# Performance work log

Measured on AMD Instinct MI355X. Metric: run time of the kernel, lower is better.

The kernel has to match this reference:

```python
import jax, jax.numpy as jnp
import numpy as np

N_NODES = 100000   # n_users + n_items
N_EDGES = 1000000  # avg degree ~10
D = 64             # embed_dim
N_LAYERS = 3


def setup_inputs() -> dict:
    key = jax.random.key(0)
    k1, k2, k3, k4 = jax.random.split(key, 4)
    embedding = jax.random.normal(k1, (N_NODES, D), dtype=jnp.float32)
    src = jax.random.randint(k2, (N_EDGES,), 0, N_NODES)
    dst = jax.random.randint(k3, (N_EDGES,), 0, N_NODES)
    # sqrt_degree is a per-node [N,1] positive scale (1/sqrt(deg) in practice)
    sqrt_degree = jax.random.uniform(k4, (N_NODES, 1), dtype=jnp.float32,
                                     minval=0.01, maxval=1.0)
    return {"embedding": embedding, "sqrt_degree": sqrt_degree,
            "src": src, "dst": dst, "n_layers": N_LAYERS}


def reference(embedding, sqrt_degree, src, dst, n_layers):
    n_nodes = embedding.shape[0]
    h = embedding
    acc = embedding  # ego embedding (layer 0)
    for _ in range(n_layers):
        # Aggregator: scale, copy_src gather, segment-sum scatter, scale
        msg = (h * sqrt_degree)[src]                                   # [E, D]
        h = jax.ops.segment_sum(msg, dst, num_segments=n_nodes)        # [N, D]
        h = h * sqrt_degree
        acc = acc + h
    # torch.mean(torch.stack(all_embed, -1), -1)
    return acc / jnp.asarray(n_layers + 1, dtype=embedding.dtype)
```

## Files before the change

### kernel.cpp

```cpp
#include <hip/hip_runtime.h>
#include <hip/hip_fp16.h>


#define N_NODES 100000
#define D 64
#define ND4 (N_NODES * D / 4)
#define SCAN_B 1024
#define NTILES ((N_NODES + SCAN_B - 1) / SCAN_B)
#define NSLICE 8
#define SLICE_DIV 12500

union H4 { uint2 u; __half2 h[2]; };
union H8 { uint4 u; __half2 h[4]; };

__global__ void init_kernel(const float4* __restrict__ emb,
                            const float* __restrict__ deg,
                            uint2* __restrict__ hs,
                            int* __restrict__ cnt, int n4) {
    int i = blockIdx.x * blockDim.x + threadIdx.x;
    if (i < N_NODES) cnt[i] = 0;
    if (i >= n4) return;
    float dg = deg[i >> 4];
    float4 v = emb[i];
    H4 x;
    x.h[0] = __float22half2_rn(make_float2(v.x * dg, v.y * dg));
    x.h[1] = __float22half2_rn(make_float2(v.z * dg, v.w * dg));
    hs[i] = x.u;
}

__global__ void hist_kernel(const int* __restrict__ dst, int* __restrict__ cnt,
                            int nedges) {
    int e = blockIdx.x * blockDim.x + threadIdx.x;
    if (e < nedges) atomicAdd(&cnt[dst[e]], 1);
}

__global__ void scanA_kernel(const int* __restrict__ cnt, int* __restrict__ off,
                             int* __restrict__ tsum, int n) {
    __shared__ int sm[SCAN_B];
    int t = threadIdx.x;
    int i = blockIdx.x * SCAN_B + t;
    int x = (i < n) ? cnt[i] : 0;
    sm[t] = x;
    __syncthreads();
    for (int o = 1; o < SCAN_B; o <<= 1) {
        int v = (t >= o) ? sm[t - o] : 0;
        __syncthreads();
        sm[t] += v;
        __syncthreads();
    }
    if (i < n) off[i] = sm[t] - x;
    if (t == SCAN_B - 1) tsum[blockIdx.x] = sm[t];
}

__global__ void scanB_kernel(int* __restrict__ tsum, int ntiles) {
    __shared__ int sm[SCAN_B];
    int t = threadIdx.x;
    int x = (t < ntiles) ? tsum[t] : 0;
    sm[t] = x;
    __syncthreads();
    for (int o = 1; o < SCAN_B; o <<= 1) {
        int v = (t >= o) ? sm[t - o] : 0;
        __syncthreads();
        sm[t] += v;
        __syncthreads();
    }
    if (t < ntiles) tsum[t] = sm[t] - x;
}

__global__ void scanC_kernel(int* __restrict__ off, const int* __restrict__ tsum,
                             int* __restrict__ cursor, int n, int nedges) {
    int i = blockIdx.x * blockDim.x + threadIdx.x;
    if (i >= n) return;
    int v = off[i] + tsum[i >> 10];
    off[i] = v;
    cursor[i] = v;
    if (i == 0) off[n] = nedges;
}

__global__ void reorder_kernel(const int* __restrict__ src,
                               const int* __restrict__ dst,
                               int* __restrict__ cursor,
                               int* __restrict__ ssrc, int nedges) {
    int slice = blockIdx.x & (NSLICE - 1);
    int e = (blockIdx.x >> 3) * blockDim.x + threadIdx.x;
    if (e >= nedges) return;
    int d = dst[e];
    if (d / SLICE_DIV != slice) return;
    int p = atomicAdd(&cursor[d], 1);
    ssrc[p] = src[e];
}

__device__ __forceinline__ void acc_h8(float* s, uint4 u) {
    H8 x; x.u = u;
    #pragma unroll
    for (int k = 0; k < 4; ++k) {
        float2 f = __half22float2(x.h[k]);
        s[2 * k]     += f.x;
        s[2 * k + 1] += f.y;
    }
}

__global__ void aggregate_kernel(const uint4* __restrict__ hs_in,
                                 const int* __restrict__ off,
                                 const int* __restrict__ ssrc,
                                 const float* __restrict__ deg,
                                 const float4* __restrict__ acc_in,
                                 float4* __restrict__ acc_out,
                                 uint4* __restrict__ hs_out,
                                 int write_hs, float scale) {
    int tid = blockIdx.x * blockDim.x + threadIdx.x;
    int n = tid >> 3;
    if (n >= N_NODES) return;
    int d8 = tid & 7;
    int start = off[n];
    int end = off[n + 1];
    float s[8] = {0.f, 0.f, 0.f, 0.f, 0.f, 0.f, 0.f, 0.f};

    int j = start;
    for (; j + 4 <= end; j += 4) {
        int ia = ssrc[j];
        int ib = ssrc[j + 1];
        int ic = ssrc[j + 2];
        int id = ssrc[j + 3];
        uint4 va = hs_in[ia * 8 + d8];
        uint4 vb = hs_in[ib * 8 + d8];
        uint4 vc = hs_in[ic * 8 + d8];
        uint4 vd = hs_in[id * 8 + d8];
        acc_h8(s, va);
        acc_h8(s, vb);
        acc_h8(s, vc);
        acc_h8(s, vd);
    }
    for (; j < end; ++j) {
        acc_h8(s, hs_in[ssrc[j] * 8 + d8]);
    }

    float dg = deg[n];
    float t[8];
    #pragma unroll
    for (int k = 0; k < 8; ++k) t[k] = s[k] * dg;

    int base = n * 16 + d8 * 2;
    float4 a0 = acc_in[base];
    float4 a1 = acc_in[base + 1];
    a0.x = (a0.x + t[0]) * scale;
    a0.y = (a0.y + t[1]) * scale;
    a0.z = (a0.z + t[2]) * scale;
    a0.w = (a0.w + t[3]) * scale;
    a1.x = (a1.x + t[4]) * scale;
    a1.y = (a1.y + t[5]) * scale;
    a1.z = (a1.z + t[6]) * scale;
    a1.w = (a1.w + t[7]) * scale;
    acc_out[base] = a0;
    acc_out[base + 1] = a1;

    if (write_hs) {
        H8 o;
        #pragma unroll
        for (int k = 0; k < 4; ++k)
            o.h[k] = __float22half2_rn(
                make_float2(t[2 * k] * dg, t[2 * k + 1] * dg));
        hs_out[tid] = o.u;
    }
}

extern "C" void kernel_launch(void* const* d_in, const int* in_sizes, int n_in,
                              void* d_out, int out_size, void* d_ws, size_t ws_size,
                              hipStream_t stream) {
    const float* emb = (const float*)d_in[0];
    const float* deg = (const float*)d_in[1];
    const int*   src = (const int*)d_in[2];
    const int*   dst = (const int*)d_in[3];
    float* out = (float*)d_out;
    int nedges = in_sizes[2];

    __half* hs_a = (__half*)d_ws;
    __half* hs_b = hs_a + (size_t)N_NODES * D;
    int*   ssrc   = (int*)(hs_b + (size_t)N_NODES * D);
    int*   cnt    = ssrc + nedges;
    int*   off    = cnt + N_NODES;
    int*   cursor = off + N_NODES + 1;
    int*   tsum   = cursor + N_NODES;

    init_kernel<<<(ND4 + 255) / 256, 256, 0, stream>>>(
        (const float4*)emb, deg, (uint2*)hs_a, cnt, ND4);
    hist_kernel<<<(nedges + 255) / 256, 256, 0, stream>>>(dst, cnt, nedges);
    scanA_kernel<<<NTILES, SCAN_B, 0, stream>>>(cnt, off, tsum, N_NODES);
    scanB_kernel<<<1, SCAN_B, 0, stream>>>(tsum, NTILES);
    scanC_kernel<<<(N_NODES + 255) / 256, 256, 0, stream>>>(
        off, tsum, cursor, N_NODES, nedges);
    reorder_kernel<<<NSLICE * ((nedges + 255) / 256), 256, 0, stream>>>(
        src, dst, cursor, ssrc, nedges);

    int nthreads = N_NODES * 8;
    int grid = (nthreads + 255) / 256;
    aggregate_kernel<<<grid, 256, 0, stream>>>(
        (const uint4*)hs_a, off, ssrc, deg, (const float4*)emb,
        (float4*)out, (uint4*)hs_b, 1, 1.0f);
    aggregate_kernel<<<grid, 256, 0, stream>>>(
        (const uint4*)hs_b, off, ssrc, deg, (const float4*)out,
        (float4*)out, (uint4*)hs_a, 1, 1.0f);
    aggregate_kernel<<<grid, 256, 0, stream>>>(
        (const uint4*)hs_a, off, ssrc, deg, (const float4*)out,
        (float4*)out, (uint4*)hs_b, 0, 0.25f);
}
```

Baseline: 259.2 us.

## Record per-edge rank during histogram to drop reorder atomics; add nontemporal hints

```diff
diff --git a/kernel.cpp b/kernel.cpp
--- a/kernel.cpp
+++ b/kernel.cpp
@@ -9,16 +9,27 @@
 #define NTILES ((N_NODES + SCAN_B - 1) / SCAN_B)
 #define NSLICE 8
 #define SLICE_DIV 12500
+#define D_MASK 0x1FFFF
+
+typedef float        f4v __attribute__((ext_vector_type(4)));
+typedef unsigned int u4v __attribute__((ext_vector_type(4)));
 
 union H4 { uint2 u; __half2 h[2]; };
-union H8 { uint4 u; __half2 h[4]; };
-
-__global__ void init_kernel(const float4* __restrict__ emb,
-                            const float* __restrict__ deg,
-                            uint2* __restrict__ hs,
-                            int* __restrict__ cnt, int n4) {
+union H8 { u4v u; __half2 h[4]; };
+
+__global__ void init_hist_kernel(const float4* __restrict__ emb,
+                                 const float* __restrict__ deg,
+                                 const int* __restrict__ dst,
+                                 uint2* __restrict__ hs,
+                                 int* __restrict__ cnt,
+                                 unsigned int* __restrict__ key,
+                                 int n4, int nedges) {
     int i = blockIdx.x * blockDim.x + threadIdx.x;
-    if (i < N_NODES) cnt[i] = 0;
+    if (i < nedges) {
+        int d = dst[i];
+        int r = atomicAdd(&cnt[d], 1);
+        key[i] = (unsigned int)d | ((unsigned int)r << 17);
+    }
     if (i >= n4) return;
     float dg = deg[i >> 4];
     float4 v = emb[i];
@@ -26,12 +37,6 @@
     x.h[0] = __float22half2_rn(make_float2(v.x * dg, v.y * dg));
     x.h[1] = __float22half2_rn(make_float2(v.z * dg, v.w * dg));
     hs[i] = x.u;
-}
-
-__global__ void hist_kernel(const int* __restrict__ dst, int* __restrict__ cnt,
-                            int nedges) {
-    int e = blockIdx.x * blockDim.x + threadIdx.x;
-    if (e < nedges) atomicAdd(&cnt[dst[e]], 1);
 }
 
 __global__ void scanA_kernel(const int* __restrict__ cnt, int* __restrict__ off,
@@ -68,29 +73,29 @@
 }
 
 __global__ void scanC_kernel(int* __restrict__ off, const int* __restrict__ tsum,
-                             int* __restrict__ cursor, int n, int nedges) {
+                             int n, int nedges) {
     int i = blockIdx.x * blockDim.x + threadIdx.x;
     if (i >= n) return;
-    int v = off[i] + tsum[i >> 10];
-    off[i] = v;
-    cursor[i] = v;
+    off[i] += tsum[i >> 10];
     if (i == 0) off[n] = nedges;
 }
 
 __global__ void reorder_kernel(const int* __restrict__ src,
-                               const int* __restrict__ dst,
-                               int* __restrict__ cursor,
+                               const unsigned int* __restrict__ key,
+                               const int* __restrict__ off,
                                int* __restrict__ ssrc, int nedges) {
     int slice = blockIdx.x & (NSLICE - 1);
     int e = (blockIdx.x >> 3) * blockDim.x + threadIdx.x;
     if (e >= nedges) return;
-    int d = dst[e];
+    unsigned int k = __builtin_nontemporal_load(&key[e]);
+    int d = (int)(k & D_MASK);
     if (d / SLICE_DIV != slice) return;
-    int p = atomicAdd(&cursor[d], 1);
-    ssrc[p] = src[e];
-}
-
-__device__ __forceinline__ void acc_h8(float* s, uint4 u) {
+    int r = (int)(k >> 17);
+    int p = off[d] + r;
+    ssrc[p] = __builtin_nontemporal_load(&src[e]);
+}
+
+__device__ __forceinline__ void acc_h8(float* s, u4v u) {
     H8 x; x.u = u;
     #pragma unroll
     for (int k = 0; k < 4; ++k) {
@@ -100,13 +105,13 @@
     }
 }
 
-__global__ void aggregate_kernel(const uint4* __restrict__ hs_in,
+__global__ void aggregate_kernel(const u4v* __restrict__ hs_in,
                                  const int* __restrict__ off,
                                  const int* __restrict__ ssrc,
                                  const float* __restrict__ deg,
-                                 const float4* __restrict__ acc_in,
-                                 float4* __restrict__ acc_out,
-                                 uint4* __restrict__ hs_out,
+                                 const f4v* __restrict__ acc_in,
+                                 f4v* __restrict__ acc_out,
+                                 u4v* __restrict__ hs_out,
                                  int write_hs, float scale) {
     int tid = blockIdx.x * blockDim.x + threadIdx.x;
     int n = tid >> 3;
@@ -117,22 +122,39 @@
     float s[8] = {0.f, 0.f, 0.f, 0.f, 0.f, 0.f, 0.f, 0.f};
 
     int j = start;
+    for (; j + 8 <= end; j += 8) {
+        int i0 = __builtin_nontemporal_load(&ssrc[j]);
+        int i1 = __builtin_nontemporal_load(&ssrc[j + 1]);
+        int i2 = __builtin_nontemporal_load(&ssrc[j + 2]);
+        int i3 = __builtin_nontemporal_load(&ssrc[j + 3]);
+        int i4 = __builtin_nontemporal_load(&ssrc[j + 4]);
+        int i5 = __builtin_nontemporal_load(&ssrc[j + 5]);
+        int i6 = __builtin_nontemporal_load(&ssrc[j + 6]);
+        int i7 = __builtin_nontemporal_load(&ssrc[j + 7]);
+        u4v v0 = hs_in[i0 * 8 + d8];
+        u4v v1 = hs_in[i1 * 8 + d8];
+        u4v v2 = hs_in[i2 * 8 + d8];
+        u4v v3 = hs_in[i3 * 8 + d8];
+        u4v v4 = hs_in[i4 * 8 + d8];
+        u4v v5 = hs_in[i5 * 8 + d8];
+        u4v v6 = hs_in[i6 * 8 + d8];
+        u4v v7 = hs_in[i7 * 8 + d8];
+        acc_h8(s, v0); acc_h8(s, v1); acc_h8(s, v2); acc_h8(s, v3);
+        acc_h8(s, v4); acc_h8(s, v5); acc_h8(s, v6); acc_h8(s, v7);
+    }
     for (; j + 4 <= end; j += 4) {
-        int ia = ssrc[j];
-        int ib = ssrc[j + 1];
-        int ic = ssrc[j + 2];
-        int id = ssrc[j + 3];
-        uint4 va = hs_in[ia * 8 + d8];
-        uint4 vb = hs_in[ib * 8 + d8];
-        uint4 vc = hs_in[ic * 8 + d8];
-        uint4 vd = hs_in[id * 8 + d8];
-        acc_h8(s, va);
-        acc_h8(s, vb);
-        acc_h8(s, vc);
-        acc_h8(s, vd);
+        int i0 = __builtin_nontemporal_load(&ssrc[j]);
+        int i1 = __builtin_nontemporal_load(&ssrc[j + 1]);
+        int i2 = __builtin_nontemporal_load(&ssrc[j + 2]);
+        int i3 = __builtin_nontemporal_load(&ssrc[j + 3]);
+        u4v v0 = hs_in[i0 * 8 + d8];
+        u4v v1 = hs_in[i1 * 8 + d8];
+        u4v v2 = hs_in[i2 * 8 + d8];
+        u4v v3 = hs_in[i3 * 8 + d8];
+        acc_h8(s, v0); acc_h8(s, v1); acc_h8(s, v2); acc_h8(s, v3);
     }
     for (; j < end; ++j) {
-        acc_h8(s, hs_in[ssrc[j] * 8 + d8]);
+        acc_h8(s, hs_in[__builtin_nontemporal_load(&ssrc[j]) * 8 + d8]);
     }
 
     float dg = deg[n];
@@ -141,8 +163,8 @@
     for (int k = 0; k < 8; ++k) t[k] = s[k] * dg;
 
     int base = n * 16 + d8 * 2;
-    float4 a0 = acc_in[base];
-    float4 a1 = acc_in[base + 1];
+    f4v a0 = __builtin_nontemporal_load(&acc_in[base]);
+    f4v a1 = __builtin_nontemporal_load(&acc_in[base + 1]);
     a0.x = (a0.x + t[0]) * scale;
     a0.y = (a0.y + t[1]) * scale;
     a0.z = (a0.z + t[2]) * scale;
@@ -151,8 +173,8 @@
     a1.y = (a1.y + t[5]) * scale;
     a1.z = (a1.z + t[6]) * scale;
     a1.w = (a1.w + t[7]) * scale;
-    acc_out[base] = a0;
-    acc_out[base + 1] = a1;
+    __builtin_nontemporal_store(a0, &acc_out[base]);
+    __builtin_nontemporal_store(a1, &acc_out[base + 1]);
 
     if (write_hs) {
         H8 o;
@@ -160,7 +182,7 @@
         for (int k = 0; k < 4; ++k)
             o.h[k] = __float22half2_rn(
                 make_float2(t[2 * k] * dg, t[2 * k + 1] * dg));
-        hs_out[tid] = o.u;
+        __builtin_nontemporal_store(o.u, &hs_out[tid]);
     }
 }
 
@@ -177,30 +199,30 @@
     __half* hs_a = (__half*)d_ws;
     __half* hs_b = hs_a + (size_t)N_NODES * D;
     int*   ssrc   = (int*)(hs_b + (size_t)N_NODES * D);
-    int*   cnt    = ssrc + nedges;
+    unsigned int* key = (unsigned int*)(ssrc + nedges);
+    int*   cnt    = (int*)(key + nedges);
     int*   off    = cnt + N_NODES;
-    int*   cursor = off + N_NODES + 1;
-    int*   tsum   = cursor + N_NODES;
-
-    init_kernel<<<(ND4 + 255) / 256, 256, 0, stream>>>(
-        (const float4*)emb, deg, (uint2*)hs_a, cnt, ND4);
-    hist_kernel<<<(nedges + 255) / 256, 256, 0, stream>>>(dst, cnt, nedges);
+    int*   tsum   = off + N_NODES + 1;
+
+    (void)hipMemsetAsync(cnt, 0, N_NODES * sizeof(int), stream);
+    init_hist_kernel<<<(ND4 + 255) / 256, 256, 0, stream>>>(
+        (const float4*)emb, deg, dst, (uint2*)hs_a, cnt, key, ND4, nedges);
     scanA_kernel<<<NTILES, SCAN_B, 0, stream>>>(cnt, off, tsum, N_NODES);
     scanB_kernel<<<1, SCAN_B, 0, stream>>>(tsum, NTILES);
     scanC_kernel<<<(N_NODES + 255) / 256, 256, 0, stream>>>(
-        off, tsum, cursor, N_NODES, nedges);
+        off, tsum, N_NODES, nedges);
     reorder_kernel<<<NSLICE * ((nedges + 255) / 256), 256, 0, stream>>>(
-        src, dst, cursor, ssrc, nedges);
+        src, key, off, ssrc, nedges);
 
     int nthreads = N_NODES * 8;
     int grid = (nthreads + 255) / 256;
     aggregate_kernel<<<grid, 256, 0, stream>>>(
-        (const uint4*)hs_a, off, ssrc, deg, (const float4*)emb,
-        (float4*)out, (uint4*)hs_b, 1, 1.0f);
+        (const u4v*)hs_a, off, ssrc, deg, (const f4v*)emb,
+        (f4v*)out, (u4v*)hs_b, 1, 1.0f);
     aggregate_kernel<<<grid, 256, 0, stream>>>(
-        (const uint4*)hs_b, off, ssrc, deg, (const float4*)out,
-        (float4*)out, (uint4*)hs_a, 1, 1.0f);
+        (const u4v*)hs_b, off, ssrc, deg, (const f4v*)out,
+        (f4v*)out, (u4v*)hs_a, 1, 1.0f);
     aggregate_kernel<<<grid, 256, 0, stream>>>(
-        (const uint4*)hs_a, off, ssrc, deg, (const float4*)out,
-        (float4*)out, (uint4*)hs_b, 0, 0.25f);
-}
+        (const u4v*)hs_a, off, ssrc, deg, (const f4v*)out,
+        (f4v*)out, (u4v*)hs_b, 0, 0.25f);
+}
```

New measurement: 251.5 us. 3.0% less time.
